# Performance work log

Hardware: AMD Instinct MI355X
Metric: run time of the kernel (lower is better)

## Reference

```python
import jax, jax.numpy as jnp
import numpy as np

N_NEURONS = 256
P_MAX = 8
N_BLOCKS = P_MAX + 1
HIDDEN = 32
BATCH = 8192


def setup_inputs() -> dict:
    key = jax.random.key(0)
    ks = jax.random.split(key, 9)
    z = jax.random.normal(ks[0], (BATCH, N_BLOCKS * N_NEURONS), dtype=jnp.float32)
    # Per-block ScalarMLP params, stacked over the n_blocks axis.
    s1 = 1.0 / np.sqrt(N_NEURONS)
    s2 = 1.0 / np.sqrt(HIDDEN)
    gW1 = jax.random.uniform(ks[1], (N_BLOCKS, N_NEURONS, HIDDEN), jnp.float32, -s1, s1)
    gb1 = jax.random.uniform(ks[2], (N_BLOCKS, HIDDEN), jnp.float32, -s1, s1)
    gW2 = jax.random.uniform(ks[3], (N_BLOCKS, HIDDEN, HIDDEN), jnp.float32, -s2, s2)
    gb2 = jax.random.uniform(ks[4], (N_BLOCKS, HIDDEN), jnp.float32, -s2, s2)
    gW3 = jax.random.uniform(ks[5], (N_BLOCKS, HIDDEN), jnp.float32, -s2, s2)
    gb3 = jax.random.uniform(ks[6], (N_BLOCKS,), jnp.float32, -s2, s2)
    # Lag coupling matrices W_r ~ U(-init_scale, init_scale), init_scale=0.1
    W = jax.random.uniform(ks[7], (P_MAX, N_NEURONS, N_NEURONS), jnp.float32, -0.1, 0.1)
    return {"z": z, "gW1": gW1, "gb1": gb1, "gW2": gW2, "gb2": gb2,
            "gW3": gW3, "gb3": gb3, "W": W}


def _energy(z, gW1, gb1, gW2, gb2, gW3, gb3, W):
    B = z.shape[0]
    blocks = z.reshape(B, N_BLOCKS, N_NEURONS)           # (B, K, n)
    # Per-block ScalarMLP energies (all blocks at once).
    h1 = jax.nn.silu(jnp.einsum('bkn,knh->bkh', blocks, gW1) + gb1)   # (B, K, H)
    h2 = jax.nn.silu(jnp.einsum('bkh,khg->bkg', h1, gW2) + gb2)       # (B, K, H)
    e = jnp.einsum('bkh,kh->bk', h2, gW3) + gb3                        # (B, K)
    # Bilinear lag couplings: z_future^T W_r z_{lag-r}, r = 1..p_max.
    z_future = blocks[:, P_MAX, :]                                     # (B, n)
    lags = blocks[:, :P_MAX, :][:, ::-1, :]                            # (B, p, n), index r-1 == block p_max-r
    cross = jnp.einsum('bi,rij,brj->b', z_future, W, lags)             # (B,)
    return e.sum(axis=-1) + cross                                      # (B,)


def reference(z, gW1, gb1, gW2, gb2, gW3, gb3, W):
    # Score s(z) = -grad_z U(z); sum over batch gives per-sample grads
    # since energies are independent across samples.
    grad_z = jax.grad(lambda zz: _energy(zz, gW1, gb1, gW2, gb2, gW3, gb3, W).sum())(z)
    return -grad_z
```

## Files before the change

### kernel.cpp

```cpp
#include <hip/hip_runtime.h>
#include <hip/hip_bf16.h>
#include <math.h>

#define BATCH 8192
#define NB 9
#define NN 256
#define PMAX 8
#define HID 32
#define ZDIM 2304

typedef short bf16x8 __attribute__((ext_vector_type(8)));
typedef float f32x4 __attribute__((ext_vector_type(4)));

static __device__ inline unsigned short f2bf(float f) {
    __hip_bfloat16 h = __float2bfloat16(f);
    return *reinterpret_cast<unsigned short*>(&h);
}

static __device__ inline uint4 pack8(float4 a, float4 b) {
    uint4 u;
    u.x = (unsigned)f2bf(a.x) | ((unsigned)f2bf(a.y) << 16);
    u.y = (unsigned)f2bf(a.z) | ((unsigned)f2bf(a.w) << 16);
    u.z = (unsigned)f2bf(b.x) | ((unsigned)f2bf(b.y) << 16);
    u.w = (unsigned)f2bf(b.z) | ((unsigned)f2bf(b.w) << 16);
    return u;
}

__global__ __launch_bounds__(256) void k_pack(
    const float* __restrict__ W, const float* __restrict__ gW1,
    unsigned short* __restrict__ Wb, unsigned short* __restrict__ WTb,
    unsigned short* __restrict__ gW1b, unsigned short* __restrict__ g1Tb) {
    int r = blockIdx.z;
    int t = threadIdx.x;
    if (r < 8) {
        __shared__ float tt[32][33];
        int i0 = blockIdx.y * 32;
        int j0 = blockIdx.x * 32;
        int tx = t & 31;
        int ty = t >> 5;
        const float* src = W + (size_t)r * 65536;
        #pragma unroll
        for (int s = 0; s < 32; s += 8) {
            float v = src[(size_t)(i0 + ty + s) * 256 + (j0 + tx)];
            tt[ty + s][tx] = v;
            Wb[(size_t)r * 65536 + (size_t)(i0 + ty + s) * 256 + (j0 + tx)] = f2bf(v);
        }
        __syncthreads();
        #pragma unroll
        for (int s = 0; s < 32; s += 8)
            WTb[(size_t)r * 65536 + (size_t)(j0 + ty + s) * 256 + (i0 + tx)] = f2bf(tt[tx][ty + s]);
    } else {
        int tg = (blockIdx.y * 8 + blockIdx.x) * 256 + t;
        for (int e = tg; e < 73728; e += 16384) {
            float v = gW1[e];
            unsigned short b = f2bf(v);
            gW1b[e] = b;
            int k = e >> 13, n = (e >> 5) & 255, h = e & 31;
            g1Tb[(size_t)(k * 32 + h) * 256 + n] = b;
        }
    }
}

__global__ __launch_bounds__(256) void k_mlp(
    const float* __restrict__ z, const unsigned short* __restrict__ g1Tb,
    const float* __restrict__ gb1, const float* __restrict__ gW2,
    const float* __restrict__ gb2, const float* __restrict__ gW3,
    float* __restrict__ d1ws, unsigned short* __restrict__ zb) {
    __shared__ uint4 As4[2][512];
    __shared__ uint4 Bw[1024];
    __shared__ uint4 W2Ts4[128];
    __shared__ uint4 W2Ns4[128];

    int t = threadIdx.x;
    int lane = t & 63;
    int w = t >> 6;
    int k = blockIdx.y;
    int b0 = blockIdx.x * 128;

    const unsigned short* bsrc = g1Tb + (size_t)k * 8192;
    for (int e = t; e < 1024; e += 256) {
        int h = e >> 5;
        int rest = e & 31;
        int c = rest >> 2, qq = rest & 3;
        Bw[c * 128 + (h & 15) + 16 * qq + 64 * (h >> 4)] =
            *(const uint4*)(bsrc + (size_t)h * 256 + c * 32 + qq * 8);
    }
    const float* gw2 = gW2 + (size_t)k * 1024;
    unsigned short* w2t = (unsigned short*)W2Ts4;
    unsigned short* w2n = (unsigned short*)W2Ns4;
    for (int e = t; e < 1024; e += 256) {
        int n = e >> 5, kk = e & 31;
        int qq = kk >> 3, jj = kk & 7;
        int ci = (n & 15) + 16 * qq + 64 * (n >> 4);
        w2t[ci * 8 + jj] = f2bf(gw2[kk * 32 + n]);
        w2n[ci * 8 + jj] = f2bf(gw2[n * 32 + kk]);
    }

    int mq = t >> 2;
    int q = t & 3;
    int ci0 = (mq & 15) + 16 * q + 64 * (mq >> 4);

    f32x4 acc1[2][2];
    #pragma unroll
    for (int i = 0; i < 2; ++i)
        #pragma unroll
        for (int j = 0; j < 2; ++j) acc1[i][j] = (f32x4){0.f, 0.f, 0.f, 0.f};

    auto loadZ = [&](int c, float4 (&fa)[2][2]) {
        #pragma unroll
        for (int pp = 0; pp < 2; ++pp) {
            int m = mq + 64 * pp;
            const float* as = z + (size_t)(b0 + m) * ZDIM + k * 256 + c * 32 + q * 8;
            fa[pp][0] = *(const float4*)(as);
            fa[pp][1] = *(const float4*)(as + 4);
        }
    };
    auto sinkZ = [&](int buf, int c, float4 (&fa)[2][2]) {
        #pragma unroll
        for (int pp = 0; pp < 2; ++pp) {
            uint4 pk = pack8(fa[pp][0], fa[pp][1]);
            As4[buf][ci0 + 256 * pp] = pk;
            int m = mq + 64 * pp;
            *(uint4*)(zb + (size_t)(b0 + m) * ZDIM + k * 256 + c * 32 + q * 8) = pk;
        }
    };

    {
        float4 fa[2][2];
        loadZ(0, fa);
        sinkZ(0, 0, fa);
    }
    int cur = 0;
    for (int c = 0; c < 8; ++c) {
        __syncthreads();
        float4 fan[2][2];
        if (c < 7) loadZ(c + 1, fan);
        bf16x8 af[2], bfr[2];
        #pragma unroll
        for (int i = 0; i < 2; ++i) af[i] = __builtin_bit_cast(bf16x8, As4[cur][lane + (w * 2 + i) * 64]);
        #pragma unroll
        for (int j = 0; j < 2; ++j) bfr[j] = __builtin_bit_cast(bf16x8, Bw[c * 128 + lane + j * 64]);
        #pragma unroll
        for (int i = 0; i < 2; ++i)
            #pragma unroll
            for (int j = 0; j < 2; ++j)
                acc1[i][j] = __builtin_amdgcn_mfma_f32_16x16x32_bf16(af[i], bfr[j], acc1[i][j], 0, 0, 0);
        if (c < 7) sinkZ(cur ^ 1, c + 1, fan);
        cur ^= 1;
    }

    int cq = lane >> 4;
    int ci16 = lane & 15;
    float b1v[2], b2v[2], g3v[2];
    #pragma unroll
    for (int j = 0; j < 2; ++j) {
        b1v[j] = gb1[k * 32 + j * 16 + ci16];
        b2v[j] = gb2[k * 32 + j * 16 + ci16];
        g3v[j] = gW3[k * 32 + j * 16 + ci16];
    }
    unsigned short* Hs = (unsigned short*)As4;
    float sp1[2][2][4];
    __syncthreads();
    #pragma unroll
    for (int i = 0; i < 2; ++i)
        #pragma unroll
        for (int j = 0; j < 2; ++j)
            #pragma unroll
            for (int r = 0; r < 4; ++r) {
                float a1 = acc1[i][j][r] + b1v[j];
                float s1 = 1.f / (1.f + __expf(-a1));
                sp1[i][j][r] = s1 * (1.f + a1 * (1.f - s1));
                int row = w * 32 + i * 16 + cq * 4 + r;
                int col = j * 16 + ci16;
                int chunk = (row & 15) + 16 * (col >> 3) + 64 * (row >> 4);
                Hs[chunk * 8 + (col & 7)] = f2bf(a1 * s1);
            }
    __syncthreads();

    bf16x8 af2[2], wf[2];
    #pragma unroll
    for (int i = 0; i < 2; ++i) af2[i] = __builtin_bit_cast(bf16x8, As4[0][lane + (w * 2 + i) * 64]);
    #pragma unroll
    for (int j = 0; j < 2; ++j) wf[j] = __builtin_bit_cast(bf16x8, W2Ts4[lane + j * 64]);
    f32x4 acc2[2][2];
    #pragma unroll
    for (int i = 0; i < 2; ++i)
        #pragma unroll
        for (int j = 0; j < 2; ++j) {
            acc2[i][j] = (f32x4){0.f, 0.f, 0.f, 0.f};
            acc2[i][j] = __builtin_amdgcn_mfma_f32_16x16x32_bf16(af2[i], wf[j], acc2[i][j], 0, 0, 0);
        }

    __syncthreads();
    #pragma unroll
    for (int i = 0; i < 2; ++i)
        #pragma unroll
        for (int j = 0; j < 2; ++j)
            #pragma unroll
            for (int r = 0; r < 4; ++r) {
                float a2 = acc2[i][j][r] + b2v[j];
                float s2 = 1.f / (1.f + __expf(-a2));
                float da2 = g3v[j] * s2 * (1.f + a2 * (1.f - s2));
                int row = w * 32 + i * 16 + cq * 4 + r;
                int col = j * 16 + ci16;
                int chunk = (row & 15) + 16 * (col >> 3) + 64 * (row >> 4);
                Hs[chunk * 8 + (col & 7)] = f2bf(da2);
            }
    __syncthreads();

    bf16x8 af3[2], wg[2];
    #pragma unroll
    for (int i = 0; i < 2; ++i) af3[i] = __builtin_bit_cast(bf16x8, As4[0][lane + (w * 2 + i) * 64]);
    #pragma unroll
    for (int j = 0; j < 2; ++j) wg[j] = __builtin_bit_cast(bf16x8, W2Ns4[lane + j * 64]);
    #pragma unroll
    for (int i = 0; i < 2; ++i)
        #pragma unroll
        for (int j = 0; j < 2; ++j) {
            f32x4 a3 = (f32x4){0.f, 0.f, 0.f, 0.f};
            a3 = __builtin_amdgcn_mfma_f32_16x16x32_bf16(af3[i], wg[j], a3, 0, 0, 0);
            #pragma unroll
            for (int r = 0; r < 4; ++r) {
                int row = w * 32 + i * 16 + cq * 4 + r;
                int col = j * 16 + ci16;
                d1ws[((size_t)k * BATCH + b0 + row) * 32 + col] = a3[r] * sp1[i][j][r];
            }
        }
}

__global__ __launch_bounds__(256) void k_gemm(
    const unsigned short* __restrict__ zb, const float* __restrict__ d1,
    const unsigned short* __restrict__ Wb, const unsigned short* __restrict__ WTb,
    const unsigned short* __restrict__ gW1b, float* __restrict__ out) {
    __shared__ uint4 As4[2][512];
    __shared__ uint4 Bs4[2][512];

    int id = blockIdx.x;
    int t = threadIdx.x;
    int lane = t & 63;
    int w = t >> 6;

    if (id < 1024) {
        int wr = w >> 1, wc = w & 1;
        int b0 = (id & 63) * 128;
        int n0 = (id >> 6) * 128;
        int k  = n0 >> 8;
        int jb = n0 & 255;

        const unsigned short* Azb = zb + (size_t)b0 * ZDIM + 2048;
        const float* Aext  = d1 + ((size_t)k * BATCH + b0) * 32;
        const unsigned short* Bmain = WTb + (size_t)(7 - k) * 65536 + (size_t)jb * 256;
        const unsigned short* Bext  = gW1b + ((size_t)k * 256 + jb) * 32;

        int mq = t >> 2;
        int q  = t & 3;
        int ci0 = (mq & 15) + 16 * q + 64 * (mq >> 4);

        auto loadAB = [&](int c, uint4 (&au)[2], uint4 (&bu)[2]) {
            #pragma unroll
            for (int pp = 0; pp < 2; ++pp) {
                int m = mq + 64 * pp;
                if (c < 8) {
                    au[pp] = *(const uint4*)(Azb + (size_t)m * ZDIM + c * 32 + q * 8);
                    bu[pp] = *(const uint4*)(Bmain + (size_t)m * 256 + c * 32 + q * 8);
                } else {
                    const float* as = Aext + (size_t)m * 32 + q * 8;
                    au[pp] = pack8(*(const float4*)(as), *(const float4*)(as + 4));
                    bu[pp] = *(const uint4*)(Bext + (size_t)m * 32 + q * 8);
                }
            }
        };
        auto storeAB = [&](int buf, uint4 (&au)[2], uint4 (&bu)[2]) {
            #pragma unroll
            for (int pp = 0; pp < 2; ++pp) {
                int idx = ci0 + 256 * pp;
                As4[buf][idx] = au[pp];
                Bs4[buf][idx] = bu[pp];
            }
        };

        f32x4 acc[4][4];
        #pragma unroll
        for (int i = 0; i < 4; ++i)
            #pragma unroll
            for (int j = 0; j < 4; ++j) acc[i][j] = (f32x4){0.f, 0.f, 0.f, 0.f};

        {
            uint4 au[2], bu[2];
            loadAB(0, au, bu);
            storeAB(0, au, bu);
        }
        int cur = 0;
        for (int c = 0; c < 9; ++c) {
            __syncthreads();
            uint4 aun[2], bun[2];
            if (c < 8) loadAB(c + 1, aun, bun);
            bf16x8 af[4], bf[4];
            #pragma unroll
            for (int i = 0; i < 4; ++i) af[i] = __builtin_bit_cast(bf16x8, As4[cur][lane + (wr * 4 + i) * 64]);
            #pragma unroll
            for (int j = 0; j < 4; ++j) bf[j] = __builtin_bit_cast(bf16x8, Bs4[cur][lane + (wc * 4 + j) * 64]);
            #pragma unroll
            for (int i = 0; i < 4; ++i)
                #pragma unroll
                for (int j = 0; j < 4; ++j)
                    acc[i][j] = __builtin_amdgcn_mfma_f32_16x16x32_bf16(af[i], bf[j], acc[i][j], 0, 0, 0);
            if (c < 8) storeAB(cur ^ 1, aun, bun);
            cur ^= 1;
        }

        int rquad = lane >> 4;
        int cidx  = lane & 15;
        #pragma unroll
        for (int i = 0; i < 4; ++i) {
            #pragma unroll
            for (int j = 0; j < 4; ++j) {
                float* o = out + (size_t)(b0 + wr * 64 + i * 16 + rquad * 4) * ZDIM
                         + (k * 256 + jb + wc * 64 + j * 16 + cidx);
                #pragma unroll
                for (int r = 0; r < 4; ++r)
                    o[(size_t)r * ZDIM] = -acc[i][j][r];
            }
        }
    } else {
        int id2 = id - 1024;
        int wr = w & 1, wc = w >> 1;
        int b0 = (id2 & 127) * 64;
        int i0 = (id2 >> 7) * 64;

        const unsigned short* Azb = zb + (size_t)b0 * ZDIM;
        const float* Aext  = d1 + ((size_t)8 * BATCH + b0) * 32;
        const unsigned short* Bext = gW1b + (size_t)(8 * 256 + i0) * 32;

        int m = t >> 2;
        int q = t & 3;
        int ci = (m & 15) + 16 * q + 64 * (m >> 4);

        auto loadAB = [&](int c, uint4 (&au)[2], uint4 (&bu)[2]) {
            if (c < 32) {
                int kb = c * 64;
                #pragma unroll
                for (int h = 0; h < 2; ++h)
                    au[h] = *(const uint4*)(Azb + (size_t)m * ZDIM + kb + h * 32 + q * 8);
                int lag = kb >> 8;
                int j0  = kb & 255;
                const unsigned short* bs = Wb + (size_t)(7 - lag) * 65536
                                             + (size_t)(i0 + m) * 256 + j0 + q * 8;
                bu[0] = *(const uint4*)(bs);
                bu[1] = *(const uint4*)(bs + 32);
            } else {
                const float* as = Aext + (size_t)m * 32 + q * 8;
                au[0] = pack8(*(const float4*)(as), *(const float4*)(as + 4));
                au[1] = make_uint4(0u, 0u, 0u, 0u);
                bu[0] = *(const uint4*)(Bext + (size_t)m * 32 + q * 8);
                bu[1] = make_uint4(0u, 0u, 0u, 0u);
            }
        };
        auto storeAB = [&](int buf, uint4 (&au)[2], uint4 (&bu)[2]) {
            #pragma unroll
            for (int h = 0; h < 2; ++h) {
                As4[buf][h * 256 + ci] = au[h];
                Bs4[buf][h * 256 + ci] = bu[h];
            }
        };

        f32x4 acc[2][2];
        #pragma unroll
        for (int i = 0; i < 2; ++i)
            #pragma unroll
            for (int j = 0; j < 2; ++j) acc[i][j] = (f32x4){0.f, 0.f, 0.f, 0.f};

        {
            uint4 au[2], bu[2];
            loadAB(0, au, bu);
            storeAB(0, au, bu);
        }
        int cur = 0;
        for (int c = 0; c < 33; ++c) {
            __syncthreads();
            uint4 aun[2], bun[2];
            if (c < 32) loadAB(c + 1, aun, bun);
            #pragma unroll
            for (int h = 0; h < 2; ++h) {
                bf16x8 af[2], bf[2];
                #pragma unroll
                for (int i = 0; i < 2; ++i)
                    af[i] = __builtin_bit_cast(bf16x8, As4[cur][h * 256 + lane + (wr * 2 + i) * 64]);
                #pragma unroll
                for (int j = 0; j < 2; ++j)
                    bf[j] = __builtin_bit_cast(bf16x8, Bs4[cur][h * 256 + lane + (wc * 2 + j) * 64]);
                #pragma unroll
                for (int i = 0; i < 2; ++i)
                    #pragma unroll
                    for (int j = 0; j < 2; ++j)
                        acc[i][j] = __builtin_amdgcn_mfma_f32_16x16x32_bf16(af[i], bf[j], acc[i][j], 0, 0, 0);
            }
            if (c < 32) storeAB(cur ^ 1, aun, bun);
            cur ^= 1;
        }

        int rquad = lane >> 4;
        int cidx  = lane & 15;
        #pragma unroll
        for (int i = 0; i < 2; ++i) {
            #pragma unroll
            for (int j = 0; j < 2; ++j) {
                float* o = out + (size_t)(b0 + wr * 32 + i * 16 + rquad * 4) * ZDIM
                         + (2048 + i0 + wc * 32 + j * 16 + cidx);
                #pragma unroll
                for (int r = 0; r < 4; ++r)
                    o[(size_t)r * ZDIM] = -acc[i][j][r];
            }
        }
    }
}

extern "C" void kernel_launch(void* const* d_in, const int* in_sizes, int n_in,
                              void* d_out, int out_size, void* d_ws, size_t ws_size,
                              hipStream_t stream) {
    const float* z   = (const float*)d_in[0];
    const float* gW1 = (const float*)d_in[1];
    const float* gb1 = (const float*)d_in[2];
    const float* gW2 = (const float*)d_in[3];
    const float* gb2 = (const float*)d_in[4];
    const float* gW3 = (const float*)d_in[5];
    const float* W   = (const float*)d_in[7];
    float* out = (float*)d_out;

    float* ws = (float*)d_ws;
    float*          d1ws = ws;
    unsigned short* Wb   = (unsigned short*)(ws + 2359296);
    unsigned short* WTb  = Wb + 524288;
    unsigned short* gW1b = WTb + 524288;
    unsigned short* g1Tb = gW1b + 73728;
    unsigned short* zb   = g1Tb + 73728;

    k_pack<<<dim3(8, 8, 9), 256, 0, stream>>>(W, gW1, Wb, WTb, gW1b, g1Tb);
    k_mlp<<<dim3(64, 9), 256, 0, stream>>>(z, g1Tb, gb1, gW2, gb2, gW3, d1ws, zb);
    k_gemm<<<dim3(1536), 256, 0, stream>>>(zb, d1ws, Wb, WTb, gW1b, out);
}
```

Baseline: 206.6 us.

## Split-K the future-block gradient GEMM into two halves with a reduction kernel

The future-block gradient blocks, which ran a 33-step K loop over all lags, are split into two K-halves of four lags each. The extra d1·gW1 term is kept in the first half. Partial results go to a workspace buffer, and a new k_red kernel sums the two halves, negates them and writes into the output. This is meant to cut the tail latency of the long-K blocks and balance them against the 128x128 blocks. In exchange it adds an extra kernel launch and an 8 MB partial write and read.

```diff
diff --git a/kernel.cpp b/kernel.cpp
--- a/kernel.cpp
+++ b/kernel.cpp
@@ -231,7 +231,8 @@
 __global__ __launch_bounds__(256) void k_gemm(
     const unsigned short* __restrict__ zb, const float* __restrict__ d1,
     const unsigned short* __restrict__ Wb, const unsigned short* __restrict__ WTb,
-    const unsigned short* __restrict__ gW1b, float* __restrict__ out) {
+    const unsigned short* __restrict__ gW1b, float* __restrict__ out,
+    float* __restrict__ Pbuf) {
     __shared__ uint4 As4[2][512];
     __shared__ uint4 Bs4[2][512];
 
@@ -326,28 +327,30 @@
         int id2 = id - 1024;
         int wr = w & 1, wc = w >> 1;
         int b0 = (id2 & 127) * 64;
-        int i0 = (id2 >> 7) * 64;
-
-        const unsigned short* Azb = zb + (size_t)b0 * ZDIM;
+        int i0 = ((id2 >> 7) & 3) * 64;
+        int s  = id2 >> 9;
+
+        const unsigned short* Azb = zb + (size_t)b0 * ZDIM + s * 1024;
         const float* Aext  = d1 + ((size_t)8 * BATCH + b0) * 32;
         const unsigned short* Bext = gW1b + (size_t)(8 * 256 + i0) * 32;
+        float* P = Pbuf + (size_t)s * (BATCH * 256);
 
         int m = t >> 2;
         int q = t & 3;
         int ci = (m & 15) + 16 * q + 64 * (m >> 4);
+        int nc = (s == 0) ? 17 : 16;
 
         auto loadAB = [&](int c, uint4 (&au)[2], uint4 (&bu)[2]) {
-            if (c < 32) {
+            if (c < 16) {
                 int kb = c * 64;
                 #pragma unroll
-                for (int h = 0; h < 2; ++h)
+                for (int h = 0; h < 2; ++h) {
                     au[h] = *(const uint4*)(Azb + (size_t)m * ZDIM + kb + h * 32 + q * 8);
-                int lag = kb >> 8;
-                int j0  = kb & 255;
-                const unsigned short* bs = Wb + (size_t)(7 - lag) * 65536
-                                             + (size_t)(i0 + m) * 256 + j0 + q * 8;
-                bu[0] = *(const uint4*)(bs);
-                bu[1] = *(const uint4*)(bs + 32);
+                    int lag = s * 4 + (c >> 2);
+                    int j0  = (kb + h * 32) & 255;
+                    bu[h] = *(const uint4*)(Wb + (size_t)(7 - lag) * 65536
+                                               + (size_t)(i0 + m) * 256 + j0 + q * 8);
+                }
             } else {
                 const float* as = Aext + (size_t)m * 32 + q * 8;
                 au[0] = pack8(*(const float4*)(as), *(const float4*)(as + 4));
@@ -376,10 +379,10 @@
             storeAB(0, au, bu);
         }
         int cur = 0;
-        for (int c = 0; c < 33; ++c) {
+        for (int c = 0; c < nc; ++c) {
             __syncthreads();
             uint4 aun[2], bun[2];
-            if (c < 32) loadAB(c + 1, aun, bun);
+            if (c < nc - 1) loadAB(c + 1, aun, bun);
             #pragma unroll
             for (int h = 0; h < 2; ++h) {
                 bf16x8 af[2], bf[2];
@@ -395,7 +398,7 @@
                     for (int j = 0; j < 2; ++j)
                         acc[i][j] = __builtin_amdgcn_mfma_f32_16x16x32_bf16(af[i], bf[j], acc[i][j], 0, 0, 0);
             }
-            if (c < 32) storeAB(cur ^ 1, aun, bun);
+            if (c < nc - 1) storeAB(cur ^ 1, aun, bun);
             cur ^= 1;
         }
 
@@ -405,14 +408,29 @@
         for (int i = 0; i < 2; ++i) {
             #pragma unroll
             for (int j = 0; j < 2; ++j) {
-                float* o = out + (size_t)(b0 + wr * 32 + i * 16 + rquad * 4) * ZDIM
-                         + (2048 + i0 + wc * 32 + j * 16 + cidx);
+                float* o = P + (size_t)(b0 + wr * 32 + i * 16 + rquad * 4) * 256
+                         + (i0 + wc * 32 + j * 16 + cidx);
                 #pragma unroll
                 for (int r = 0; r < 4; ++r)
-                    o[(size_t)r * ZDIM] = -acc[i][j][r];
-            }
-        }
-    }
+                    o[(size_t)r * 256] = acc[i][j][r];
+            }
+        }
+    }
+}
+
+__global__ __launch_bounds__(256) void k_red(
+    const float* __restrict__ Pbuf, float* __restrict__ out) {
+    int idx = blockIdx.x * 256 + threadIdx.x;
+    float4 a = *(const float4*)(Pbuf + (size_t)idx * 4);
+    float4 b = *(const float4*)(Pbuf + (size_t)BATCH * 256 + (size_t)idx * 4);
+    int row = idx >> 6;
+    int jj  = (idx & 63) * 4;
+    float4 o;
+    o.x = -(a.x + b.x);
+    o.y = -(a.y + b.y);
+    o.z = -(a.z + b.z);
+    o.w = -(a.w + b.w);
+    *(float4*)(out + (size_t)row * ZDIM + 2048 + jj) = o;
 }
 
 extern "C" void kernel_launch(void* const* d_in, const int* in_sizes, int n_in,
@@ -434,8 +452,10 @@
     unsigned short* gW1b = WTb + 524288;
     unsigned short* g1Tb = gW1b + 73728;
     unsigned short* zb   = g1Tb + 73728;
+    float*          Pbuf = (float*)(zb + 18874368);
 
     k_pack<<<dim3(8, 8, 9), 256, 0, stream>>>(W, gW1, Wb, WTb, gW1b, g1Tb);
     k_mlp<<<dim3(64, 9), 256, 0, stream>>>(z, g1Tb, gb1, gW2, gb2, gW3, d1ws, zb);
-    k_gemm<<<dim3(1536), 256, 0, stream>>>(zb, d1ws, Wb, WTb, gW1b, out);
-}
+    k_gemm<<<dim3(2048), 256, 0, stream>>>(zb, d1ws, Wb, WTb, gW1b, out, Pbuf);
+    k_red<<<dim3(2048), 256, 0, stream>>>(Pbuf, out);
+}
```

Result: no change. 208.2 us (+0.8%).
